# Performance work log

Measured on AMD Instinct MI355X. Metric: run time of the kernel, lower is better.

Reference implementation:

```python
import jax, jax.numpy as jnp
import numpy as np

# Module hyperparameters (from init_kwargs)
DEPTH = 4
SMOOTH_STEP_PARAM = 1.0
TREES_NUM = 16
INPUT_DIM = 2048
OUTPUT_DIM = 512
BATCH = 8192
NUM_LEAVES = 2 ** DEPTH          # 16
NUM_INTERNAL = NUM_LEAVES - 1    # 15


def _routing_matrix():
    """R[n, l] = +1 if leaf l is in the left subtree of node n (gate = s),
    -1 if in the right subtree (gate = 1 - s), 0 if node n not on leaf l's path.
    Node indexing: root = 0, children of n are 2n+1 (left), 2n+2 (right)."""
    R = np.zeros((NUM_INTERNAL, NUM_LEAVES), dtype=np.float32)
    for l in range(NUM_LEAVES):
        node = 0
        for lvl in range(DEPTH):
            bit = (l >> (DEPTH - 1 - lvl)) & 1  # 0 = go left, 1 = go right
            R[node, l] = 1.0 if bit == 0 else -1.0
            node = 2 * node + 1 + bit
    return R

ROUTE = jnp.asarray(_routing_matrix())  # [NUM_INTERNAL, NUM_LEAVES]


def smooth_step(v):
    # TEL smooth-step: t = clip(ssp * v + 0.5, 0, 1); s = -2t^3 + 3t^2
    t = jnp.clip(SMOOTH_STEP_PARAM * v + 0.5, 0.0, 1.0)
    return t * t * (3.0 - 2.0 * t)


def setup_inputs() -> dict:
    key = jax.random.key(0)
    k1, k2, k3 = jax.random.split(key, 3)
    x = jax.random.normal(k1, (BATCH, INPUT_DIM), dtype=jnp.float32)
    node_weights = jax.random.normal(k2, (TREES_NUM, INPUT_DIM, NUM_INTERNAL), dtype=jnp.float32) * 0.02
    leaf_weights = jax.random.normal(k3, (TREES_NUM, OUTPUT_DIM, NUM_LEAVES), dtype=jnp.float32) * 0.02
    return {"x": x, "node_weights": node_weights, "leaf_weights": leaf_weights}


def reference(x, node_weights, leaf_weights):
    # Node pre-activations for all trees: [B, T, NUM_INTERNAL]
    a = jnp.einsum('bi,tin->btn', x, node_weights)
    s = smooth_step(a)  # probability of routing LEFT at each internal node
    left = (ROUTE == 1.0)
    right = (ROUTE == -1.0)
    # Per-(node, leaf) routing factor; nodes off the path contribute 1.
    terms = jnp.where(left, s[..., None], jnp.where(right, 1.0 - s[..., None], 1.0))  # [B,T,NI,NL]
    leaf_prob = jnp.prod(terms, axis=2)  # [B, T, NUM_LEAVES]
    # Weighted leaf aggregation, summed over trees (sum_outputs=True)
    out = jnp.einsum('btl,tol->bo', leaf_prob, leaf_weights)  # [B, OUTPUT_DIM]
    return out
```

## Files before the change

kernel.cpp:

```cpp
#include <hip/hip_runtime.h>
#include <cstdint>
#include <cstddef>

typedef __fp16 half8 __attribute__((ext_vector_type(8)));
typedef float  f32x4 __attribute__((ext_vector_type(4)));

#define BATCH 8192
#define INDIM 2048
#define OUTD  512
#define NC    256
#define BM    32
#define BK    128

__device__ __forceinline__ half8 cvt8(float4 a, float4 b) {
  half8 h;
  h[0] = (__fp16)a.x; h[1] = (__fp16)a.y; h[2] = (__fp16)a.z; h[3] = (__fp16)a.w;
  h[4] = (__fp16)b.x; h[5] = (__fp16)b.y; h[6] = (__fp16)b.z; h[7] = (__fp16)b.w;
  return h;
}

__global__ void kprepW(const float* __restrict__ nw, __fp16* __restrict__ WrT) {
  int idx = blockIdx.x * 256 + threadIdx.x;
  int c  = idx >> 7;
  int k0 = (idx & 127) * 16;
  int t = c >> 4, n = c & 15;
  half8 lo = {}, hi = {};
  if (n < 15) {
    const float* src = nw + (size_t)t * INDIM * 15 + n;
    #pragma unroll
    for (int j = 0; j < 8; j++) lo[j] = (__fp16)src[(size_t)(k0 + j) * 15];
    #pragma unroll
    for (int j = 0; j < 8; j++) hi[j] = (__fp16)src[(size_t)(k0 + 8 + j) * 15];
  }
  *(half8*)(WrT + (size_t)c * INDIM + k0)     = lo;
  *(half8*)(WrT + (size_t)c * INDIM + k0 + 8) = hi;
}

__global__ void kprepL(const float* __restrict__ lw, __fp16* __restrict__ LWrT) {
  int idx = blockIdx.x * 256 + threadIdx.x;
  int o = idx >> 4;
  int t = idx & 15;
  const float* src = lw + ((size_t)t * OUTD + o) * 16;
  half8 lo, hi;
  #pragma unroll
  for (int j = 0; j < 8; j++) lo[j] = (__fp16)src[j];
  #pragma unroll
  for (int j = 0; j < 8; j++) hi[j] = (__fp16)src[8 + j];
  *(half8*)(LWrT + (size_t)o * NC + t * 16)     = lo;
  *(half8*)(LWrT + (size_t)o * NC + t * 16 + 8) = hi;
}

__global__ __launch_bounds__(512, 2)
void kfused(const float* __restrict__ x, const __fp16* __restrict__ WrT,
            const __fp16* __restrict__ LWrT, float* __restrict__ out) {
  __shared__ char   uni[BM * NC * 4];
  __shared__ __fp16 Ps[BM * NC];
  __fp16* Xs = (__fp16*)uni;
  float*  As = (float*)uni;

  const int tid  = threadIdx.x;
  const int lane = tid & 63;
  const int wv   = tid >> 6;
  const int l15  = lane & 15;
  const int lg   = lane >> 4;
  const int r0   = blockIdx.x * BM;
  const int sr   = tid >> 4;
  const int sk   = tid & 15;
  const int sOff = (sr * BK + sk * 8) ^ ((sr & 7) << 3);

  {
    const float* xp = x + (size_t)(r0 + sr) * INDIM + sk * 8;
    float4 a = *(const float4*)xp;
    float4 b = *(const float4*)(xp + 4);
    *(half8*)&Xs[sOff] = cvt8(a, b);
  }

  f32x4 acc1[2][2] = {};
  const __fp16* wbase = WrT + (size_t)(32 * wv + l15) * INDIM + lg * 8;

  for (int ch = 0; ch < INDIM / BK; ++ch) {
    const int cur = ch & 1;
    float4 a, b;
    const bool more = (ch + 1 < INDIM / BK);
    if (more) {
      const float* xp = x + (size_t)(r0 + sr) * INDIM + (ch + 1) * BK + sk * 8;
      a = *(const float4*)xp;
      b = *(const float4*)(xp + 4);
    }
    half8 bf[2][4];
    #pragma unroll
    for (int nt = 0; nt < 2; nt++)
      #pragma unroll
      for (int ks = 0; ks < 4; ks++)
        bf[nt][ks] = *(const half8*)(wbase + (size_t)nt * 16 * INDIM + ch * BK + ks * 32);

    __syncthreads();

    #pragma unroll
    for (int ks = 0; ks < 4; ks++) {
      half8 af[2];
      #pragma unroll
      for (int mt = 0; mt < 2; mt++) {
        const int r = l15 + 16 * mt;
        const int e = (r * BK + ks * 32 + lg * 8) ^ ((r & 7) << 3);
        af[mt] = *(const half8*)&Xs[cur * (BM * BK) + e];
      }
      #pragma unroll
      for (int mt = 0; mt < 2; mt++)
        #pragma unroll
        for (int nt = 0; nt < 2; nt++)
          acc1[mt][nt] = __builtin_amdgcn_mfma_f32_16x16x32_f16(af[mt], bf[nt][ks], acc1[mt][nt], 0, 0, 0);
    }
    if (more)
      *(half8*)&Xs[(cur ^ 1) * (BM * BK) + sOff] = cvt8(a, b);
  }

  __syncthreads();

  #pragma unroll
  for (int mt = 0; mt < 2; mt++)
    #pragma unroll
    for (int nt = 0; nt < 2; nt++)
      #pragma unroll
      for (int i = 0; i < 4; i++)
        As[(16 * mt + 4 * lg + i) * NC + 32 * wv + 16 * nt + l15] = acc1[mt][nt][i];
  __syncthreads();

  {
    const int row = tid >> 4, tr = tid & 15;
    float av[16];
    #pragma unroll
    for (int q = 0; q < 4; q++) {
      f32x4 v = *(const f32x4*)&As[row * NC + tr * 16 + 4 * q];
      av[4 * q + 0] = v[0]; av[4 * q + 1] = v[1];
      av[4 * q + 2] = v[2]; av[4 * q + 3] = v[3];
    }
    float sg[15];
    #pragma unroll
    for (int m = 0; m < 15; m++) {
      float t = fminf(fmaxf(av[m] + 0.5f, 0.f), 1.f);
      sg[m] = t * t * (3.f - 2.f * t);
    }
    float p[16];
    #pragma unroll
    for (int l = 0; l < 16; l++) {
      float pr = 1.f; int node = 0;
      #pragma unroll
      for (int L = 0; L < 4; L++) {
        int bit = (l >> (3 - L)) & 1;
        pr *= bit ? (1.f - sg[node]) : sg[node];
        node = 2 * node + 1 + bit;
      }
      p[l] = pr;
    }
    half8 h0, h1;
    #pragma unroll
    for (int j = 0; j < 8; j++) { h0[j] = (__fp16)p[j]; h1[j] = (__fp16)p[8 + j]; }
    const int base = row * NC + tr * 16;
    const int swz  = (row & 7) << 3;
    *(half8*)&Ps[(base) ^ swz]     = h0;
    *(half8*)&Ps[(base + 8) ^ swz] = h1;
  }
  __syncthreads();

  f32x4 acc2[2][4] = {};
  const __fp16* lbase = LWrT + (size_t)(64 * wv + l15) * NC + lg * 8;
  #pragma unroll
  for (int kc = 0; kc < 2; kc++) {
    half8 bf2[4][4];
    #pragma unroll
    for (int nt = 0; nt < 4; nt++)
      #pragma unroll
      for (int ks = 0; ks < 4; ks++)
        bf2[nt][ks] = *(const half8*)(lbase + (size_t)nt * 16 * NC + kc * 128 + ks * 32);
    #pragma unroll
    for (int ks = 0; ks < 4; ks++) {
      half8 af[2];
      #pragma unroll
      for (int mt = 0; mt < 2; mt++) {
        const int r = l15 + 16 * mt;
        const int e = (r * NC + kc * 128 + ks * 32 + lg * 8) ^ ((r & 7) << 3);
        af[mt] = *(const half8*)&Ps[e];
      }
      #pragma unroll
      for (int mt = 0; mt < 2; mt++)
        #pragma unroll
        for (int nt = 0; nt < 4; nt++)
          acc2[mt][nt] = __builtin_amdgcn_mfma_f32_16x16x32_f16(af[mt], bf2[nt][ks], acc2[mt][nt], 0, 0, 0);
    }
  }
  #pragma unroll
  for (int mt = 0; mt < 2; mt++)
    #pragma unroll
    for (int nt = 0; nt < 4; nt++)
      #pragma unroll
      for (int i = 0; i < 4; i++)
        out[(size_t)(r0 + 16 * mt + 4 * lg + i) * OUTD + 64 * wv + 16 * nt + l15] = acc2[mt][nt][i];
}

extern "C" void kernel_launch(void* const* d_in, const int* in_sizes, int n_in,
                              void* d_out, int out_size, void* d_ws, size_t ws_size,
                              hipStream_t stream) {
  const float* x  = (const float*)d_in[0];
  const float* nw = (const float*)d_in[1];
  const float* lw = (const float*)d_in[2];
  float* out = (float*)d_out;

  __fp16* WrT  = (__fp16*)d_ws;
  __fp16* LWrT = (__fp16*)((char*)d_ws + (size_t)NC * INDIM * 2);

  hipLaunchKernelGGL(kprepW, dim3(128), dim3(256), 0, stream, nw, WrT);
  hipLaunchKernelGGL(kprepL, dim3(32),  dim3(256), 0, stream, lw, LWrT);
  hipLaunchKernelGGL(kfused, dim3(BATCH / BM), dim3(512), 0, stream, x, WrT, LWrT, out);
}
```

Before: 137.1 us.

## Deepen main-loop prefetch, coalesce weight prep via LDS transpose, relax launch bounds

The first GEMM loop is unrolled by two. It holds two register sets of node-weight fragments and prefetches x two chunks ahead, so global loads overlap more MFMA work. kprepW now stages a tile of node weights in shared memory so that global reads are coalesced before the transpose to fp16. kprepL uses float4 loads. The fused kernel's launch bounds drop from 2 to 1 blocks per CU minimum, which frees registers for the extra prefetch buffers but may lower occupancy.

```diff
diff --git a/kernel.cpp b/kernel.cpp
--- a/kernel.cpp
+++ b/kernel.cpp
@@ -11,6 +11,7 @@
 #define NC    256
 #define BM    32
 #define BK    128
+#define NCH   (INDIM / BK)
 
 __device__ __forceinline__ half8 cvt8(float4 a, float4 b) {
   half8 h;
@@ -19,38 +20,49 @@
   return h;
 }
 
-__global__ void kprepW(const float* __restrict__ nw, __fp16* __restrict__ WrT) {
-  int idx = blockIdx.x * 256 + threadIdx.x;
-  int c  = idx >> 7;
-  int k0 = (idx & 127) * 16;
-  int t = c >> 4, n = c & 15;
-  half8 lo = {}, hi = {};
+__global__ __launch_bounds__(256)
+void kprepW(const float* __restrict__ nw, __fp16* __restrict__ WrT) {
+  __shared__ float Ls[128][16];
+  const int tid = threadIdx.x;
+  const int t  = blockIdx.x >> 4;
+  const int k0 = (blockIdx.x & 15) * 128;
+  const float* base = nw + ((size_t)t * INDIM + k0) * 15;
+  #pragma unroll
+  for (int i = 0; i < 8; i++) {
+    int fl = tid + 256 * i;
+    if (fl < 1920) {
+      float v = base[fl];
+      int kk = (int)(((unsigned)fl * 8739u) >> 17);
+      int n  = fl - 15 * kk;
+      Ls[kk][n] = v;
+    }
+  }
+  __syncthreads();
+  const int n  = tid >> 4;
+  const int kc = tid & 15;
+  half8 h = {};
   if (n < 15) {
-    const float* src = nw + (size_t)t * INDIM * 15 + n;
-    #pragma unroll
-    for (int j = 0; j < 8; j++) lo[j] = (__fp16)src[(size_t)(k0 + j) * 15];
-    #pragma unroll
-    for (int j = 0; j < 8; j++) hi[j] = (__fp16)src[(size_t)(k0 + 8 + j) * 15];
-  }
-  *(half8*)(WrT + (size_t)c * INDIM + k0)     = lo;
-  *(half8*)(WrT + (size_t)c * INDIM + k0 + 8) = hi;
-}
-
-__global__ void kprepL(const float* __restrict__ lw, __fp16* __restrict__ LWrT) {
-  int idx = blockIdx.x * 256 + threadIdx.x;
-  int o = idx >> 4;
-  int t = idx & 15;
+    #pragma unroll
+    for (int j = 0; j < 8; j++) h[j] = (__fp16)Ls[kc * 8 + j][n];
+  }
+  *(half8*)(WrT + (size_t)(16 * t + n) * INDIM + k0 + kc * 8) = h;
+}
+
+__global__ __launch_bounds__(256)
+void kprepL(const float* __restrict__ lw, __fp16* __restrict__ LWrT) {
+  int g = blockIdx.x * 256 + threadIdx.x;
+  int o = g >> 4;
+  int t = g & 15;
   const float* src = lw + ((size_t)t * OUTD + o) * 16;
-  half8 lo, hi;
-  #pragma unroll
-  for (int j = 0; j < 8; j++) lo[j] = (__fp16)src[j];
-  #pragma unroll
-  for (int j = 0; j < 8; j++) hi[j] = (__fp16)src[8 + j];
-  *(half8*)(LWrT + (size_t)o * NC + t * 16)     = lo;
-  *(half8*)(LWrT + (size_t)o * NC + t * 16 + 8) = hi;
-}
-
-__global__ __launch_bounds__(512, 2)
+  float4 a = *(const float4*)(src);
+  float4 b = *(const float4*)(src + 4);
+  float4 c = *(const float4*)(src + 8);
+  float4 d = *(const float4*)(src + 12);
+  *(half8*)(LWrT + (size_t)o * NC + t * 16)     = cvt8(a, b);
+  *(half8*)(LWrT + (size_t)o * NC + t * 16 + 8) = cvt8(c, d);
+}
+
+__global__ __launch_bounds__(512, 1)
 void kfused(const float* __restrict__ x, const __fp16* __restrict__ WrT,
             const __fp16* __restrict__ LWrT, float* __restrict__ out) {
   __shared__ char   uni[BM * NC * 4];
@@ -68,51 +80,55 @@
   const int sk   = tid & 15;
   const int sOff = (sr * BK + sk * 8) ^ ((sr & 7) << 3);
 
-  {
-    const float* xp = x + (size_t)(r0 + sr) * INDIM + sk * 8;
-    float4 a = *(const float4*)xp;
-    float4 b = *(const float4*)(xp + 4);
-    *(half8*)&Xs[sOff] = cvt8(a, b);
-  }
+  const float* xrow = x + (size_t)(r0 + sr) * INDIM + sk * 8;
+  const __fp16* wbase = WrT + (size_t)(32 * wv + l15) * INDIM + lg * 8;
 
   f32x4 acc1[2][2] = {};
-  const __fp16* wbase = WrT + (size_t)(32 * wv + l15) * INDIM + lg * 8;
-
-  for (int ch = 0; ch < INDIM / BK; ++ch) {
-    const int cur = ch & 1;
-    float4 a, b;
-    const bool more = (ch + 1 < INDIM / BK);
-    if (more) {
-      const float* xp = x + (size_t)(r0 + sr) * INDIM + (ch + 1) * BK + sk * 8;
-      a = *(const float4*)xp;
-      b = *(const float4*)(xp + 4);
-    }
-    half8 bf[2][4];
-    #pragma unroll
-    for (int nt = 0; nt < 2; nt++)
-      #pragma unroll
-      for (int ks = 0; ks < 4; ks++)
-        bf[nt][ks] = *(const half8*)(wbase + (size_t)nt * 16 * INDIM + ch * BK + ks * 32);
-
+
+  half8 bfA[2][4], bfB[2][4];
+  float4 xN0, xN1, xM0, xM1;
+
+  #define LDB(dst, ch)                                                          \
+    _Pragma("unroll") for (int nt = 0; nt < 2; nt++)                            \
+    _Pragma("unroll") for (int ks = 0; ks < 4; ks++)                            \
+      dst[nt][ks] = *(const half8*)(wbase + (size_t)nt * 16 * INDIM + (ch) * BK + ks * 32);
+
+  #define LDX(d0, d1, ch)                                                       \
+    d0 = *(const float4*)(xrow + (ch) * BK);                                    \
+    d1 = *(const float4*)(xrow + (ch) * BK + 4);
+
+  #define STX(buf, d0, d1)                                                      \
+    *(half8*)&Xs[(buf) * (BM * BK) + sOff] = cvt8(d0, d1);
+
+  #define COMPUTE(buf, bf)                                                      \
+    _Pragma("unroll") for (int ks = 0; ks < 4; ks++) {                          \
+      half8 af[2];                                                              \
+      _Pragma("unroll") for (int mt = 0; mt < 2; mt++) {                        \
+        const int r = l15 + 16 * mt;                                            \
+        const int e = (r * BK + ks * 32 + lg * 8) ^ ((r & 7) << 3);             \
+        af[mt] = *(const half8*)&Xs[(buf) * (BM * BK) + e];                     \
+      }                                                                         \
+      _Pragma("unroll") for (int mt = 0; mt < 2; mt++)                          \
+      _Pragma("unroll") for (int nt = 0; nt < 2; nt++)                          \
+        acc1[mt][nt] = __builtin_amdgcn_mfma_f32_16x16x32_f16(af[mt], bf[nt][ks], acc1[mt][nt], 0, 0, 0); \
+    }
+
+  { float4 a, b; LDX(a, b, 0); STX(0, a, b); }
+  LDX(xN0, xN1, 1);
+  LDB(bfA, 0);
+
+  #pragma unroll 1
+  for (int ch = 0; ch < NCH; ch += 2) {
+    LDB(bfB, ch + 1);
+    if (ch + 2 < NCH) { LDX(xM0, xM1, ch + 2); }
     __syncthreads();
-
-    #pragma unroll
-    for (int ks = 0; ks < 4; ks++) {
-      half8 af[2];
-      #pragma unroll
-      for (int mt = 0; mt < 2; mt++) {
-        const int r = l15 + 16 * mt;
-        const int e = (r * BK + ks * 32 + lg * 8) ^ ((r & 7) << 3);
-        af[mt] = *(const half8*)&Xs[cur * (BM * BK) + e];
-      }
-      #pragma unroll
-      for (int mt = 0; mt < 2; mt++)
-        #pragma unroll
-        for (int nt = 0; nt < 2; nt++)
-          acc1[mt][nt] = __builtin_amdgcn_mfma_f32_16x16x32_f16(af[mt], bf[nt][ks], acc1[mt][nt], 0, 0, 0);
-    }
-    if (more)
-      *(half8*)&Xs[(cur ^ 1) * (BM * BK) + sOff] = cvt8(a, b);
+    STX(1, xN0, xN1);
+    COMPUTE(0, bfA);
+    if (ch + 2 < NCH) { LDB(bfA, ch + 2); }
+    if (ch + 3 < NCH) { LDX(xN0, xN1, ch + 3); }
+    __syncthreads();
+    if (ch + 2 < NCH) { STX(0, xM0, xM1); }
+    COMPUTE(1, bfB);
   }
 
   __syncthreads();
@@ -209,7 +225,7 @@
   __fp16* WrT  = (__fp16*)d_ws;
   __fp16* LWrT = (__fp16*)((char*)d_ws + (size_t)NC * INDIM * 2);
 
-  hipLaunchKernelGGL(kprepW, dim3(128), dim3(256), 0, stream, nw, WrT);
+  hipLaunchKernelGGL(kprepW, dim3(256), dim3(256), 0, stream, nw, WrT);
   hipLaunchKernelGGL(kprepL, dim3(32),  dim3(256), 0, stream, lw, LWrT);
   hipLaunchKernelGGL(kfused, dim3(BATCH / BM), dim3(512), 0, stream, x, WrT, LWrT, out);
 }
```

Result: no change. 137.1 us (-0.0%).
